# Kernel optimization log

Hardware: AMD Instinct MI355X
Metric: run time of the kernel (lower is better)

## Reference

```python
import jax, jax.numpy as jnp
import numpy as np
from jax import lax

IMG = 224
KS = 7
NS = 7
PAD = (KS // 2) * 2  # 6, max_scale=2


def _windows():
    # Replicates COGV1.__init__ geometry (torch.linspace + int truncation)
    scales = np.linspace(2.0, 1.0, NS, dtype=np.float32)
    borders = np.linspace(0, IMG // 2, NS + 1).astype(int)
    wins = []
    for s in range(NS):
        a = int(borders[s]); b = int(borders[s + 1])
        c = IMG - b; d = IMG - a
        # top, left, bottom, right windows of the hollow square
        for (t, l, bo, r) in [(a, a, b, c), (b, a, d, b), (c, b, d, d), (a, c, c, d)]:
            h = bo - t; w = r - l
            # padded window size / scale, truncated toward zero (torch .int())
            sh = int(np.float32(h + 2 * PAD) / scales[s])
            sw = int(np.float32(w + 2 * PAD) / scales[s])
            wins.append((t, l, bo, r, h, w, sh, sw))
    return wins

WINS = _windows()


def _nearest_up(f, H, W):
    # torch nearest: src_idx = floor(dst_idx * in / out); static indices
    hin, win = f.shape[-2], f.shape[-1]
    ih = (np.arange(H) * hin) // H
    iw = (np.arange(W) * win) // W
    return f[..., ih[:, None], iw[None, :]]


def _bn(x, g, b, eps=1e-5):
    # training-mode BatchNorm2d: per-batch biased stats over (N,H,W)
    m = jnp.mean(x, axis=(0, 2, 3), keepdims=True)
    v = jnp.mean((x - m) ** 2, axis=(0, 2, 3), keepdims=True)
    return (x - m) * lax.rsqrt(v + eps) * g[:, None, None] + b[:, None, None]


def _conv(x, w, padding):
    return lax.conv_general_dilated(x, w, (1, 1), padding,
                                    dimension_numbers=('NCHW', 'OIHW', 'NCHW'))


def setup_inputs() -> dict:
    key = jax.random.key(0)
    ks = jax.random.split(key, 3)
    B = 16
    return {
        'inp': jax.random.normal(ks[0], (B, 3, IMG, IMG), jnp.float32),
        'conv1_w': jax.random.normal(ks[1], (128, 3, KS, KS), jnp.float32) * 0.05,
        'gamma1': jnp.ones((128,), jnp.float32),
        'beta1': jnp.zeros((128,), jnp.float32),
        'conv2_w': jax.random.normal(ks[2], (128, 128, 3, 3), jnp.float32) * 0.05,
        'gamma2': jnp.ones((128,), jnp.float32),
        'beta2': jnp.zeros((128,), jnp.float32),
    }


def reference(inp, conv1_w, gamma1, beta1, conv2_w, gamma2, beta2):
    B = inp.shape[0]
    xp = jnp.pad(inp, ((0, 0), (0, 0), (PAD, PAD), (PAD, PAD)))  # ConstantPad2d(6)
    out = jnp.zeros((B, 128, IMG, IMG), inp.dtype)
    for (t, l, bo, r, h, w, sh, sw) in WINS:
        win = xp[:, :, t:bo + 2 * PAD, l:r + 2 * PAD]
        # antialiased bilinear downsample (== torch bilinear antialias=True)
        xd = jax.image.resize(win, (B, 3, sh, sw), method='linear', antialias=True)
        f = _conv(xd, conv1_w, 'VALID')  # 7x7 valid conv
        out = out.at[:, :, t:bo, l:r].set(_nearest_up(f, h, w))
    x = jax.nn.relu(_bn(out, gamma1, beta1))
    # MaxPool2d(kernel=3, stride=2, padding=1): 224 -> 112
    x = lax.reduce_window(x, -jnp.inf, lax.max, (1, 1, 3, 3), (1, 1, 2, 2),
                          ((0, 0), (0, 0), (1, 1), (1, 1)))
    x = _conv(x, conv2_w, ((1, 1), (1, 1)))  # 3x3 same conv
    return jax.nn.relu(_bn(x, gamma2, beta2))
```

## Files before the change

### kernel.cpp

```cpp
#include <hip/hip_runtime.h>
#include <stdint.h>

#define NW 28
#define IMG 224
#define XD_TOTAL 1822272
#define POOL_ELEMS 26615808
#define OUT_ELEMS 25690112

#define XD_OFF_B    0
#define POOL_OFF_B  3644928
#define W1P_OFF_B   56876544
#define W2T_OFF_B   56925696
#define STATS_OFF_B 57220608
#define TAB_OUT_OFF_B 93667328

typedef __attribute__((ext_vector_type(8))) short short8;
typedef __attribute__((ext_vector_type(4))) float f32x4;

#define WIN_TABLE(W) \
  W(  0,  0, 16,208, 14,110,       0,        0,    0, 7) \
  W( 16,  0,208, 16,110, 14,   73920,  1703936,  112, 7) \
  W(208, 16, 16,208, 14,110,  147840,  3407872,  224, 7) \
  W(  0,208,208, 16,110, 14,  221760,  5111808,  336, 7) \
  W( 16, 16, 16,176, 15,102,  295680,  6815744,  448, 7) \
  W( 32, 16,176, 16,102, 15,  369120,  8585216,  560, 7) \
  W(192, 32, 16,176, 15,102,  442560, 10354688,  672, 7) \
  W( 16,192,176, 16,102, 15,  516000, 12124160,  784, 7) \
  W( 32, 32, 16,144, 16, 93,  589440, 13893632,  896, 7) \
  W( 48, 32,144, 16, 93, 16,  660864, 15675392, 1008, 7) \
  W(176, 48, 16,144, 16, 93,  732288, 17457152, 1120, 7) \
  W( 32,176,144, 16, 93, 16,  803712, 19238912, 1232, 7) \
  W( 48, 48, 16,112, 18, 82,  875136, 21020672, 1344, 8) \
  W( 64, 48,112, 16, 82, 18,  945984, 22888448, 1472, 8) \
  W(160, 64, 16,112, 18, 82, 1016832, 24756224, 1600, 8) \
  W( 48,160,112, 16, 82, 18, 1087680, 26624000, 1728, 8) \
  W( 64, 64, 16, 80, 21, 69, 1158528, 28491776, 1856, 8) \
  W( 80, 64, 80, 16, 69, 21, 1228080, 30427136, 1984, 8) \
  W(144, 80, 16, 80, 21, 69, 1297632, 32362496, 2112, 8) \
  W( 64,144, 80, 16, 69, 21, 1367184, 34297856, 2240, 8) \
  W( 80, 80, 16, 48, 24, 51, 1436736, 36233216, 2368, 7) \
  W( 96, 80, 48, 16, 51, 24, 1495488, 37892096, 2480, 7) \
  W(128, 96, 16, 48, 24, 51, 1554240, 39550976, 2592, 7) \
  W( 80,128, 48, 16, 51, 24, 1612992, 41209856, 2704, 7) \
  W( 96, 96, 16, 16, 28, 28, 1671744, 42868736, 2816, 4) \
  W(112, 96, 16, 16, 28, 28, 1709376, 43859968, 2880, 4) \
  W(112,112, 16, 16, 28, 28, 1747008, 44851200, 2944, 4) \
  W( 96,112, 16, 16, 28, 28, 1784640, 45842432, 3008, 4)

#define GT(t,l,h,ww,sh,sw,xdo,fo,ts,tpb) (t),
#define GL(t,l,h,ww,sh,sw,xdo,fo,ts,tpb) (l),
#define GH(t,l,h,ww,sh,sw,xdo,fo,ts,tpb) (h),
#define GW(t,l,h,ww,sh,sw,xdo,fo,ts,tpb) (ww),
#define GSH(t,l,h,ww,sh,sw,xdo,fo,ts,tpb) (sh),
#define GSW(t,l,h,ww,sh,sw,xdo,fo,ts,tpb) (sw),
#define GXO(t,l,h,ww,sh,sw,xdo,fo,ts,tpb) (xdo),
#define GFO(t,l,h,ww,sh,sw,xdo,fo,ts,tpb) (fo),
#define GTS(t,l,h,ww,sh,sw,xdo,fo,ts,tpb) (ts),
#define GTPB(t,l,h,ww,sh,sw,xdo,fo,ts,tpb) (tpb),
#define GXE(t,l,h,ww,sh,sw,xdo,fo,ts,tpb) ((xdo) + 48*(sh)*(sw)),
#define GTE(t,l,h,ww,sh,sw,xdo,fo,ts,tpb) ((ts) + 16*(tpb)),
#define GIH(t,l,h,ww,sh,sw,xdo,fo,ts,tpb) (1.0f/(float)(h)),
#define GIW(t,l,h,ww,sh,sw,xdo,fo,ts,tpb) (1.0f/(float)(ww)),
#define GIFW(t,l,h,ww,sh,sw,xdo,fo,ts,tpb) (1.0f/(float)((sw)-6)),
#define GRSY(t,l,h,ww,sh,sw,xdo,fo,ts,tpb) ((float)((h)+12)/(float)(sh)),
#define GRSX(t,l,h,ww,sh,sw,xdo,fo,ts,tpb) ((float)((ww)+12)/(float)(sw)),
#define GI3(t,l,h,ww,sh,sw,xdo,fo,ts,tpb) (1.0f/(float)(3*(sh)*(sw))),
#define GISS(t,l,h,ww,sh,sw,xdo,fo,ts,tpb) (1.0f/(float)((sh)*(sw))),
#define GISW(t,l,h,ww,sh,sw,xdo,fo,ts,tpb) (1.0f/(float)(sw)),

__constant__ int   W_T[NW]     = { WIN_TABLE(GT) };
__constant__ int   W_L[NW]     = { WIN_TABLE(GL) };
__constant__ int   W_H[NW]     = { WIN_TABLE(GH) };
__constant__ int   W_WW[NW]    = { WIN_TABLE(GW) };
__constant__ int   W_SH[NW]    = { WIN_TABLE(GSH) };
__constant__ int   W_SW[NW]    = { WIN_TABLE(GSW) };
__constant__ int   W_XDOFF[NW] = { WIN_TABLE(GXO) };
__constant__ int   W_FOFF[NW]  = { WIN_TABLE(GFO) };
__constant__ int   W_TSTART[NW]= { WIN_TABLE(GTS) };
__constant__ int   W_TPB[NW]   = { WIN_TABLE(GTPB) };
__constant__ int   W_XDEND[NW] = { WIN_TABLE(GXE) };
__constant__ int   W_TEND[NW]  = { WIN_TABLE(GTE) };
__constant__ float W_INVH[NW]  = { WIN_TABLE(GIH) };
__constant__ float W_INVW[NW]  = { WIN_TABLE(GIW) };
__constant__ float W_INVFW[NW] = { WIN_TABLE(GIFW) };
__constant__ float W_RSY[NW]   = { WIN_TABLE(GRSY) };
__constant__ float W_RSX[NW]   = { WIN_TABLE(GRSX) };
__constant__ float W_INV3[NW]  = { WIN_TABLE(GI3) };
__constant__ float W_INVSS[NW] = { WIN_TABLE(GISS) };
__constant__ float W_INVSW[NW] = { WIN_TABLE(GISW) };

__device__ __forceinline__ float bf2f(uint16_t h) {
  union { uint32_t u; float f; } v; v.u = ((uint32_t)h) << 16; return v.f;
}
__device__ __forceinline__ uint16_t f2bf(float x) {
  union { float f; uint32_t u; } v; v.f = x;
  uint32_t r = v.u + 0x7FFFu + ((v.u >> 16) & 1u);
  return (uint16_t)(r >> 16);
}

__global__ void k_prep(const float* __restrict__ w1, const float* __restrict__ w2,
                       uint16_t* __restrict__ w1p, uint16_t* __restrict__ w2f) {
  int i = blockIdx.x * 256 + threadIdx.x;
  if (i < 128 * 192) {
    int cout = i / 192, k = i - cout * 192;
    int chunk = k >> 3, kx = k & 7;
    float v = 0.f;
    if (chunk < 21 && kx < 7) {
      int ch = chunk / 7, ky = chunk - ch * 7;
      v = w1[((cout * 3 + ch) * 7 + ky) * 7 + kx];
    }
    w1p[i] = f2bf(v);
  }
  int j2 = i - 128 * 192;
  if (j2 >= 0 && j2 < 128 * 1152) {
    int e    = j2 & 7;
    int lane = (j2 >> 3) & 63;
    int jj   = (j2 >> 9) & 3;
    int half = (j2 >> 11) & 1;
    int kk   = j2 >> 12;
    int cout = half * 64 + jj * 16 + (lane & 15);
    int k    = kk * 32 + ((lane >> 4) << 3) + e;
    int tap = k >> 7, ci = k & 127;
    int ty = tap / 3, tx = tap - ty * 3;
    w2f[j2] = f2bf(w2[((cout * 128 + ci) * 3 + ty) * 3 + tx]);
  }
}

__global__ void k_tapoff(int2* __restrict__ tab) {
  int i = blockIdx.x * 256 + threadIdx.x;
  if (i >= IMG * IMG) return;
  int y = i / IMG, x = i - y * IMG;
  int dmin = min(min(y, 223 - y), min(x, 223 - x));
  int s = dmin >> 4; if (s > 6) s = 6;
  int b2 = (s << 4) + 16, cc = 208 - (s << 4);
  int side;
  if (y < b2) side = (x < cc) ? 0 : 3;
  else if (y >= cc) side = (x >= b2) ? 2 : 1;
  else side = (x < b2) ? 1 : 3;
  int w = (s << 2) + side;
  int fh = W_SH[w] - 6, fw = W_SW[w] - 6;
  int fy = (int)(((float)((y - W_T[w]) * fh) + 0.5f) * W_INVH[w]);
  int fx = (int)(((float)((x - W_L[w]) * fw) + 0.5f) * W_INVW[w]);
  tab[i] = make_int2(W_FOFF[w] + (fy * fw + fx) * 128, fh * fw * 128);
}

__global__ void k_resize(const float* __restrict__ inp, uint16_t* __restrict__ xd) {
  int idx = blockIdx.x * 256 + threadIdx.x;
  if (idx >= XD_TOTAL) return;
  int w = 0;
  while (w < NW - 1 && idx >= W_XDEND[w]) w++;
  int rem = idx - W_XDOFF[w];
  int sh = W_SH[w], sw = W_SW[w];
  int shsw = sh * sw;
  int b  = (int)(((float)rem + 0.5f) * W_INV3[w]);
  int r2 = rem - b * 3 * shsw;
  int ch = (int)(((float)r2 + 0.5f) * W_INVSS[w]);
  int r3 = r2 - ch * shsw;
  int oy = (int)(((float)r3 + 0.5f) * W_INVSW[w]);
  int ox = r3 - oy * sw;
  int t = W_T[w], l = W_L[w], h = W_H[w], ww = W_WW[w];
  int hiny = h + 12, hinx = ww + 12;
  float rsy = W_RSY[w], rsx = W_RSX[w];
  float iky = 1.0f / rsy, ikx = 1.0f / rsx;
  float sfy = ((float)oy + 0.5f) * rsy - 0.5f;
  float sfx = ((float)ox + 0.5f) * rsx - 0.5f;
  int y0 = (int)ceilf(sfy - rsy); if (y0 < 0) y0 = 0;
  int y1 = (int)floorf(sfy + rsy); if (y1 > hiny - 1) y1 = hiny - 1;
  int x0 = (int)ceilf(sfx - rsx); if (x0 < 0) x0 = 0;
  int x1 = (int)floorf(sfx + rsx); if (x1 > hinx - 1) x1 = hinx - 1;
  float wy[4], wx[4], sy = 0.f, sx = 0.f;
  #pragma unroll
  for (int k = 0; k < 4; k++) {
    int iy = y0 + k;
    float a = (iy <= y1) ? fmaxf(0.f, 1.f - fabsf((float)iy - sfy) * iky) : 0.f;
    wy[k] = a; sy += a;
    int ix = x0 + k;
    float a2 = (ix <= x1) ? fmaxf(0.f, 1.f - fabsf((float)ix - sfx) * ikx) : 0.f;
    wx[k] = a2; sx += a2;
  }
  const float* src = inp + (b * 3 + ch) * IMG * IMG;
  float accv = 0.f;
  #pragma unroll
  for (int ky = 0; ky < 4; ky++) {
    int gy = t + y0 + ky - 6;
    if (wy[ky] > 0.f && gy >= 0 && gy < IMG) {
      float rowa = 0.f;
      #pragma unroll
      for (int kx = 0; kx < 4; kx++) {
        int gx = l + x0 + kx - 6;
        if (wx[kx] > 0.f && gx >= 0 && gx < IMG)
          rowa += wx[kx] * src[gy * IMG + gx];
      }
      accv += wy[ky] * rowa;
    }
  }
  xd[idx] = f2bf(accv / (sy * sx));
}

__global__ void k_conv1(const uint16_t* __restrict__ xd,
                        const uint16_t* __restrict__ w1p,
                        uint16_t* __restrict__ f) {
  __shared__ short8 As[512];
  __shared__ short8 Bs[512];
  int bid = blockIdx.x;
  int w = 0;
  while (w < NW - 1 && bid >= W_TEND[w]) w++;
  int rel = bid - W_TSTART[w];
  int tpb = W_TPB[w];
  int b  = rel / tpb;
  int mt = rel - b * tpb;
  int m0 = mt << 7;
  int sh = W_SH[w], sw = W_SW[w];
  int fh = sh - 6, fw = sw - 6;
  int fhfw = fh * fw;
  float invfw = W_INVFW[w];
  int xdo = W_XDOFF[w];
  int fo  = W_FOFF[w];
  int tid = threadIdx.x;
  int lane = tid & 63, wv = tid >> 6;
  int mn = tid & 127, q0 = tid >> 7;

  int pm0 = m0 + mn; if (pm0 > fhfw - 1) pm0 = fhfw - 1;
  int fy0 = (int)(((float)pm0 + 0.5f) * invfw);
  int fx0 = pm0 - fy0 * fw;
  const uint16_t* arow = xd + xdo + (b * 3) * sh * sw;
  const uint16_t* brow = w1p + mn * 192;

  f32x4 acc[4][4];
  #pragma unroll
  for (int i = 0; i < 4; i++)
    #pragma unroll
    for (int j = 0; j < 4; j++)
      acc[i][j] = (f32x4){0.f, 0.f, 0.f, 0.f};

  for (int kk = 0; kk < 6; kk++) {
    short8 av[2], bv[2];
    #pragma unroll
    for (int j = 0; j < 2; j++) {
      int q = (j << 1) | q0;
      int gc = (kk << 2) + q;
      const uint16_t* src;
      if (gc < 21) {
        int ch = gc / 7, ky = gc - ch * 7;
        src = arow + (ch * sh + fy0 + ky) * sw + fx0;
      } else {
        src = xd;
      }
      short8 pk;
      pk[0]=(short)src[0]; pk[1]=(short)src[1]; pk[2]=(short)src[2]; pk[3]=(short)src[3];
      pk[4]=(short)src[4]; pk[5]=(short)src[5]; pk[6]=(short)src[6]; pk[7]=(short)src[7];
      av[j] = pk;
      bv[j] = *(const short8*)(brow + (kk << 5) + (q << 3));
    }
    __syncthreads();
    #pragma unroll
    for (int j = 0; j < 2; j++) {
      int ck = (j << 8) + tid;
      As[ck] = av[j];
      Bs[ck] = bv[j];
    }
    __syncthreads();
    int q = lane >> 4, ln = lane & 15;
    int wmB = (wv >> 1) << 6, wnB = (wv & 1) << 6;
    short8 af[4], bfr[4];
    #pragma unroll
    for (int i = 0; i < 4; i++) af[i]  = As[(q << 7) + wmB + (i << 4) + ln];
    #pragma unroll
    for (int j = 0; j < 4; j++) bfr[j] = Bs[(q << 7) + wnB + (j << 4) + ln];
    #pragma unroll
    for (int i = 0; i < 4; i++)
      #pragma unroll
      for (int j = 0; j < 4; j++)
        acc[i][j] = __builtin_amdgcn_mfma_f32_16x16x32_bf16(af[i], bfr[j], acc[i][j], 0, 0, 0);
  }

  int q = lane >> 4, ln = lane & 15;
  int wmB = (wv >> 1) << 6, wnB = (wv & 1) << 6;
  int base = fo + b * fhfw * 128;
  #pragma unroll
  for (int i = 0; i < 4; i++) {
    #pragma unroll
    for (int j = 0; j < 4; j++) {
      int n = wnB + (j << 4) + ln;
      int mrow = m0 + wmB + (i << 4) + (q << 2);
      #pragma unroll
      for (int r = 0; r < 4; r++) {
        int pm = mrow + r;
        if (pm < fhfw) f[base + pm * 128 + n] = f2bf(acc[i][j][r]);
      }
    }
  }
}

__global__ void k_stats1(const uint16_t* __restrict__ f, float* __restrict__ sums) {
  __shared__ float cwt[960];
  __shared__ float sS[128], sQ[128];
  int w = blockIdx.x;
  int b = blockIdx.y;
  int sh = W_SH[w], sw = W_SW[w];
  int fh = sh - 6, fw = sw - 6, fhfw = fh * fw;
  int h = W_H[w], ww = W_WW[w];
  int tid = threadIdx.x;
  if (tid < 128) { sS[tid] = 0.f; sQ[tid] = 0.f; }
  for (int e = tid; e < fhfw; e += 1024) {
    int fy = e / fw, fx = e - fy * fw;
    int cy = ((fy + 1) * h + fh - 1) / fh - (fy * h + fh - 1) / fh;
    int cx = ((fx + 1) * ww + fw - 1) / fw - (fx * ww + fw - 1) / fw;
    cwt[e] = (float)(cy * cx);
  }
  __syncthreads();
  int c = tid & 127, eh = tid >> 7;
  int base = W_FOFF[w] + b * fhfw * 128;
  float s = 0.f, q2 = 0.f;
  for (int e = eh; e < fhfw; e += 8) {
    float v = bf2f(f[base + e * 128 + c]);
    float cw = cwt[e];
    s += v * cw; q2 += v * v * cw;
  }
  atomicAdd(&sS[c], s);
  atomicAdd(&sQ[c], q2);
  __syncthreads();
  if (tid < 128) {
    atomicAdd(&sums[tid], sS[tid]);
    atomicAdd(&sums[128 + tid], sQ[tid]);
  }
}

__global__ void k_bnparam(const float* __restrict__ sums,
                          const float* __restrict__ gamma, const float* __restrict__ beta,
                          float n, float* __restrict__ scale, float* __restrict__ bias) {
  int c = threadIdx.x;
  float mean = sums[c] / n;
  float var = sums[128 + c] / n - mean * mean;
  var = fmaxf(var, 0.f);
  float sc = gamma[c] / sqrtf(var + 1e-5f);
  scale[c] = sc;
  bias[c] = beta[c] - mean * sc;
}

__global__ void k_maxpool(const uint16_t* __restrict__ f,
                          const float* __restrict__ scale, const float* __restrict__ bias,
                          const int2* __restrict__ tab,
                          uint16_t* __restrict__ pooled) {
  int tid = threadIdx.x;
  int g = blockIdx.x * 16 + (tid >> 4);
  int c0 = (tid & 15) << 3;
  int xx = g % 114;
  int r  = g / 114;
  int yy = r % 114;
  int bb = r / 114;
  short8 outv = (short8){0,0,0,0,0,0,0,0};
  if (yy >= 1 && yy <= 112 && xx >= 1 && xx <= 112) {
    float m[8];
    #pragma unroll
    for (int k = 0; k < 8; k++) m[k] = -1e30f;
    int py = yy - 1, px = xx - 1;
    #pragma unroll
    for (int dy = 0; dy < 3; dy++) {
      int y = 2 * py - 1 + dy;
      if (y < 0) continue;
      #pragma unroll
      for (int dx = 0; dx < 3; dx++) {
        int x = 2 * px - 1 + dx;
        if (x < 0) continue;
        int2 t = tab[y * IMG + x];
        short8 v = *(const short8*)(f + t.x + bb * t.y + c0);
        #pragma unroll
        for (int k = 0; k < 8; k++) m[k] = fmaxf(m[k], bf2f((uint16_t)v[k]));
      }
    }
    f32x4 s0 = *(const f32x4*)(scale + c0);
    f32x4 s1 = *(const f32x4*)(scale + c0 + 4);
    f32x4 b0 = *(const f32x4*)(bias + c0);
    f32x4 b1 = *(const f32x4*)(bias + c0 + 4);
    #pragma unroll
    for (int k = 0; k < 4; k++) {
      outv[k]     = (short)f2bf(fmaxf(m[k]     * s0[k] + b0[k], 0.f));
      outv[k + 4] = (short)f2bf(fmaxf(m[k + 4] * s1[k] + b1[k], 0.f));
    }
  }
  *(short8*)(pooled + (size_t)g * 128 + c0) = outv;
}

__global__ void k_conv2(const uint16_t* __restrict__ pooled,
                        const uint16_t* __restrict__ w2f,
                        float* __restrict__ out, float* __restrict__ sums) {
  __shared__ float sS[128], sQ[128];
  int bid = blockIdx.x;
  int b = bid / 98;
  int m0 = bid << 7;
  int local0 = m0 - b * 12544;
  int tid = threadIdx.x;
  int lane = tid & 63, wv = tid >> 6;
  int q = lane >> 4, ln = lane & 15;
  int wmB = (wv >> 1) << 6;
  int half = wv & 1;
  int wnB = half << 6;
  if (tid < 128) { sS[tid] = 0.f; sQ[tid] = 0.f; }

  const uint16_t* ap = pooled + (size_t)b * 114 * 114 * 128;
  int rowoff[4];
  #pragma unroll
  for (int i = 0; i < 4; i++) {
    int pm = local0 + wmB + (i << 4) + ln;
    int yp = pm / 112, xp = pm - yp * 112;
    rowoff[i] = (yp * 114 + xp) * 128;
  }

  f32x4 acc[4][4];
  #pragma unroll
  for (int i = 0; i < 4; i++)
    #pragma unroll
    for (int j = 0; j < 4; j++)
      acc[i][j] = (f32x4){0.f, 0.f, 0.f, 0.f};

  const uint16_t* bbase = w2f + (half << 11) + (lane << 3);

  #pragma unroll
  for (int tap = 0; tap < 9; tap++) {
    const int ty = tap / 3, tx = tap - ty * 3;
    int tbase = (ty * 114 + tx) * 128 + (q << 3);
    #pragma unroll
    for (int cc = 0; cc < 4; cc++) {
      int kk = (tap << 2) + cc;
      int c0 = cc << 5;
      short8 af[4], bfr[4];
      #pragma unroll
      for (int i = 0; i < 4; i++)
        af[i] = *(const short8*)(ap + rowoff[i] + tbase + c0);
      #pragma unroll
      for (int j = 0; j < 4; j++)
        bfr[j] = *(const short8*)(bbase + (kk << 12) + (j << 9));
      #pragma unroll
      for (int i = 0; i < 4; i++)
        #pragma unroll
        for (int j = 0; j < 4; j++)
          acc[i][j] = __builtin_amdgcn_mfma_f32_16x16x32_bf16(af[i], bfr[j], acc[i][j], 0, 0, 0);
    }
  }

  #pragma unroll
  for (int i = 0; i < 4; i++) {
    #pragma unroll
    for (int j = 0; j < 4; j++) {
      int n = wnB + (j << 4) + ln;
      int prow = local0 + wmB + (i << 4) + (q << 2);
      float* dst = out + (size_t)(b * 128 + n) * 12544 + prow;
      *(f32x4*)dst = acc[i][j];
    }
  }
  __syncthreads();
  #pragma unroll
  for (int j = 0; j < 4; j++) {
    int n = wnB + (j << 4) + ln;
    float s = 0.f, q2 = 0.f;
    #pragma unroll
    for (int i = 0; i < 4; i++)
      #pragma unroll
      for (int r = 0; r < 4; r++) {
        float v = acc[i][j][r];
        s += v; q2 += v * v;
      }
    atomicAdd(&sS[n], s);
    atomicAdd(&sQ[n], q2);
  }
  __syncthreads();
  if (tid < 128) {
    atomicAdd(&sums[tid], sS[tid]);
    atomicAdd(&sums[128 + tid], sQ[tid]);
  }
}

__global__ void k_final(f32x4* __restrict__ out,
                        const float* __restrict__ scale, const float* __restrict__ bias) {
  int i = blockIdx.x * 256 + threadIdx.x;
  int c = (i / 3136) & 127;
  f32x4 v = out[i];
  float sc = scale[c], bi = bias[c];
  #pragma unroll
  for (int k = 0; k < 4; k++) v[k] = fmaxf(v[k] * sc + bi, 0.f);
  out[i] = v;
}

extern "C" void kernel_launch(void* const* d_in, const int* in_sizes, int n_in,
                              void* d_out, int out_size, void* d_ws, size_t ws_size,
                              hipStream_t stream) {
  (void)in_sizes; (void)n_in; (void)out_size; (void)ws_size;
  const float* inp = (const float*)d_in[0];
  const float* w1  = (const float*)d_in[1];
  const float* g1  = (const float*)d_in[2];
  const float* b1  = (const float*)d_in[3];
  const float* w2  = (const float*)d_in[4];
  const float* g2  = (const float*)d_in[5];
  const float* b2  = (const float*)d_in[6];
  float* out = (float*)d_out;
  char* ws = (char*)d_ws;
  uint16_t* xd     = (uint16_t*)(ws + XD_OFF_B);
  uint16_t* pooled = (uint16_t*)(ws + POOL_OFF_B);
  uint16_t* w1p    = (uint16_t*)(ws + W1P_OFF_B);
  uint16_t* w2f    = (uint16_t*)(ws + W2T_OFF_B);
  float* stats  = (float*)(ws + STATS_OFF_B);
  int2*  tab    = (int2*)((char*)d_out + TAB_OUT_OFF_B);
  float* sums1  = stats;
  float* sums2  = stats + 256;
  float* scale1 = stats + 512;
  float* bias1  = stats + 640;
  float* scale2 = stats + 768;
  float* bias2  = stats + 896;
  uint16_t* f = (uint16_t*)d_out;

  hipMemsetAsync(stats, 0, 2048, stream);
  k_prep   <<<dim3(672),        dim3(256),  0, stream>>>(w1, w2, w1p, w2f);
  k_tapoff <<<dim3(196),        dim3(256),  0, stream>>>(tab);
  k_resize <<<dim3(7119),       dim3(256),  0, stream>>>(inp, xd);
  k_conv1  <<<dim3(3072),       dim3(256),  0, stream>>>(xd, w1p, f);
  k_stats1 <<<dim3(28, 16),     dim3(1024), 0, stream>>>(f, sums1);
  k_bnparam<<<dim3(1),          dim3(128),  0, stream>>>(sums1, g1, b1, 802816.0f, scale1, bias1);
  k_maxpool<<<dim3(12996),      dim3(256),  0, stream>>>(f, scale1, bias1, tab, pooled);
  k_conv2  <<<dim3(1568),       dim3(256),  0, stream>>>(pooled, w2f, out, sums2);
  k_bnparam<<<dim3(1),          dim3(128),  0, stream>>>(sums2, g2, b2, 200704.0f, scale2, bias2);
  k_final  <<<dim3(25088),      dim3(256),  0, stream>>>((f32x4*)out, scale2, bias2);
}
```

Before: 494.9 us.

## Stage conv2 A/B tiles into swizzled LDS via direct global-to-LDS loads

The 3x3 conv2 kernel no longer has each wave load its A (pooled activation) and B (weight) fragments straight from global memory. Each tap's 128x128 A tile and 128x128 B tile are now staged into XOR-swizzled shared memory with global_load_lds, so every element is fetched from global once per block and shared across waves. The weight prep kernel is rewritten to emit the matching swizzled layout, and the LDS used for the BN partial sums is reused. The kernel uses 64KB of LDS and adds two barriers per tap without double buffering, which can limit occupancy and leave load latency exposed.

```diff
diff --git a/kernel.cpp b/kernel.cpp
--- a/kernel.cpp
+++ b/kernel.cpp
@@ -16,6 +16,10 @@
 
 typedef __attribute__((ext_vector_type(8))) short short8;
 typedef __attribute__((ext_vector_type(4))) float f32x4;
+
+#define GLD16(gp, lp) __builtin_amdgcn_global_load_lds( \
+    (const __attribute__((address_space(1))) void*)(gp), \
+    (__attribute__((address_space(3))) void*)(lp), 16, 0, 0)
 
 #define WIN_TABLE(W) \
   W(  0,  0, 16,208, 14,110,       0,        0,    0, 7) \
@@ -99,7 +103,7 @@
 }
 
 __global__ void k_prep(const float* __restrict__ w1, const float* __restrict__ w2,
-                       uint16_t* __restrict__ w1p, uint16_t* __restrict__ w2f) {
+                       uint16_t* __restrict__ w1p, uint16_t* __restrict__ w2s) {
   int i = blockIdx.x * 256 + threadIdx.x;
   if (i < 128 * 192) {
     int cout = i / 192, k = i - cout * 192;
@@ -112,17 +116,14 @@
     w1p[i] = f2bf(v);
   }
   int j2 = i - 128 * 192;
-  if (j2 >= 0 && j2 < 128 * 1152) {
-    int e    = j2 & 7;
-    int lane = (j2 >> 3) & 63;
-    int jj   = (j2 >> 9) & 3;
-    int half = (j2 >> 11) & 1;
-    int kk   = j2 >> 12;
-    int cout = half * 64 + jj * 16 + (lane & 15);
-    int k    = kk * 32 + ((lane >> 4) << 3) + e;
-    int tap = k >> 7, ci = k & 127;
+  if (j2 >= 0 && j2 < 147456) {
+    int e   = j2 & 7;
+    int cc  = (j2 >> 3) & 15;
+    int n   = (j2 >> 7) & 127;
+    int tap = j2 >> 14;
+    int ci  = ((cc ^ (n & 15)) << 3) + e;
     int ty = tap / 3, tx = tap - ty * 3;
-    w2f[j2] = f2bf(w2[((cout * 128 + ci) * 3 + ty) * 3 + tx]);
+    w2s[j2] = f2bf(w2[((n * 128 + ci) * 3 + ty) * 3 + tx]);
   }
 }
 
@@ -382,10 +383,12 @@
   *(short8*)(pooled + (size_t)g * 128 + c0) = outv;
 }
 
-__global__ void k_conv2(const uint16_t* __restrict__ pooled,
-                        const uint16_t* __restrict__ w2f,
+__global__ __launch_bounds__(256) void k_conv2(
+                        const uint16_t* __restrict__ pooled,
+                        const uint16_t* __restrict__ w2s,
                         float* __restrict__ out, float* __restrict__ sums) {
-  __shared__ float sS[128], sQ[128];
+  __shared__ short8 As[2048];
+  __shared__ short8 Bs[2048];
   int bid = blockIdx.x;
   int b = bid / 98;
   int m0 = bid << 7;
@@ -393,18 +396,19 @@
   int tid = threadIdx.x;
   int lane = tid & 63, wv = tid >> 6;
   int q = lane >> 4, ln = lane & 15;
-  int wmB = (wv >> 1) << 6;
-  int half = wv & 1;
-  int wnB = half << 6;
-  if (tid < 128) { sS[tid] = 0.f; sQ[tid] = 0.f; }
-
-  const uint16_t* ap = pooled + (size_t)b * 114 * 114 * 128;
-  int rowoff[4];
-  #pragma unroll
-  for (int i = 0; i < 4; i++) {
-    int pm = local0 + wmB + (i << 4) + ln;
-    int yp = pm / 112, xp = pm - yp * 112;
-    rowoff[i] = (yp * 114 + xp) * 128;
+  int wmB = (wv >> 1) << 6, wnB = (wv & 1) << 6;
+  const char* apc = (const char*)(pooled + (size_t)b * 114 * 114 * 128);
+
+  int slot0 = (wv << 9) + lane;
+  int rowbyte[8];
+  #pragma unroll
+  for (int r = 0; r < 8; r++) {
+    int slot = slot0 + (r << 6);
+    int pix = slot >> 4;
+    int cc = slot & 15;
+    int loc = local0 + pix;
+    int yp = loc / 112, xp = loc - yp * 112;
+    rowbyte[r] = ((yp * 114 + xp) << 8) + ((cc ^ (pix & 15)) << 4);
   }
 
   f32x4 acc[4][4];
@@ -414,29 +418,35 @@
     for (int j = 0; j < 4; j++)
       acc[i][j] = (f32x4){0.f, 0.f, 0.f, 0.f};
 
-  const uint16_t* bbase = w2f + (half << 11) + (lane << 3);
-
   #pragma unroll
   for (int tap = 0; tap < 9; tap++) {
     const int ty = tap / 3, tx = tap - ty * 3;
-    int tbase = (ty * 114 + tx) * 128 + (q << 3);
-    #pragma unroll
-    for (int cc = 0; cc < 4; cc++) {
-      int kk = (tap << 2) + cc;
-      int c0 = cc << 5;
+    const int tapoff = (ty * 114 + tx) << 8;
+    const uint16_t* gb = w2s + (tap << 14) + (slot0 << 3);
+    #pragma unroll
+    for (int r = 0; r < 8; r++) {
+      int slot = slot0 + (r << 6);
+      GLD16(apc + tapoff + rowbyte[r], &As[slot]);
+      GLD16(gb + (r << 9), &Bs[slot]);
+    }
+    __syncthreads();
+    #pragma unroll
+    for (int kk2 = 0; kk2 < 4; kk2++) {
+      int cq = (kk2 << 2) + q;
       short8 af[4], bfr[4];
       #pragma unroll
       for (int i = 0; i < 4; i++)
-        af[i] = *(const short8*)(ap + rowoff[i] + tbase + c0);
+        af[i] = As[((wmB + (i << 4) + ln) << 4) + (cq ^ ln)];
       #pragma unroll
       for (int j = 0; j < 4; j++)
-        bfr[j] = *(const short8*)(bbase + (kk << 12) + (j << 9));
+        bfr[j] = Bs[((wnB + (j << 4) + ln) << 4) + (cq ^ ln)];
       #pragma unroll
       for (int i = 0; i < 4; i++)
         #pragma unroll
         for (int j = 0; j < 4; j++)
           acc[i][j] = __builtin_amdgcn_mfma_f32_16x16x32_bf16(af[i], bfr[j], acc[i][j], 0, 0, 0);
     }
+    __syncthreads();
   }
 
   #pragma unroll
@@ -449,6 +459,9 @@
       *(f32x4*)dst = acc[i][j];
     }
   }
+  float* sS = (float*)&As[0];
+  float* sQ = sS + 128;
+  if (tid < 128) { sS[tid] = 0.f; sQ[tid] = 0.f; }
   __syncthreads();
   #pragma unroll
   for (int j = 0; j < 4; j++) {
@@ -498,7 +511,7 @@
   uint16_t* xd     = (uint16_t*)(ws + XD_OFF_B);
   uint16_t* pooled = (uint16_t*)(ws + POOL_OFF_B);
   uint16_t* w1p    = (uint16_t*)(ws + W1P_OFF_B);
-  uint16_t* w2f    = (uint16_t*)(ws + W2T_OFF_B);
+  uint16_t* w2s    = (uint16_t*)(ws + W2T_OFF_B);
   float* stats  = (float*)(ws + STATS_OFF_B);
   int2*  tab    = (int2*)((char*)d_out + TAB_OUT_OFF_B);
   float* sums1  = stats;
@@ -510,14 +523,14 @@
   uint16_t* f = (uint16_t*)d_out;
 
   hipMemsetAsync(stats, 0, 2048, stream);
-  k_prep   <<<dim3(672),        dim3(256),  0, stream>>>(w1, w2, w1p, w2f);
+  k_prep   <<<dim3(672),        dim3(256),  0, stream>>>(w1, w2, w1p, w2s);
   k_tapoff <<<dim3(196),        dim3(256),  0, stream>>>(tab);
   k_resize <<<dim3(7119),       dim3(256),  0, stream>>>(inp, xd);
   k_conv1  <<<dim3(3072),       dim3(256),  0, stream>>>(xd, w1p, f);
   k_stats1 <<<dim3(28, 16),     dim3(1024), 0, stream>>>(f, sums1);
   k_bnparam<<<dim3(1),          dim3(128),  0, stream>>>(sums1, g1, b1, 802816.0f, scale1, bias1);
   k_maxpool<<<dim3(12996),      dim3(256),  0, stream>>>(f, scale1, bias1, tab, pooled);
-  k_conv2  <<<dim3(1568),       dim3(256),  0, stream>>>(pooled, w2f, out, sums2);
+  k_conv2  <<<dim3(1568),       dim3(256),  0, stream>>>(pooled, w2s, out, sums2);
   k_bnparam<<<dim3(1),          dim3(128),  0, stream>>>(sums2, g2, b2, 200704.0f, scale2, bias2);
   k_final  <<<dim3(25088),      dim3(256),  0, stream>>>((f32x4*)out, scale2, bias2);
 }
```

Measured after the change: 414.9 us. -16.2%, faster.
